# Kernel tuning notes

Measured on AMD Instinct MI355X. Metric: run time of the kernel, lower is better.

## Reference

```python
import jax, jax.numpy as jnp
import numpy as np


def lstm_encode(x, Wih, Whh, b):
    """x: [S, T, F] -> final hidden state [S, H]. PyTorch LSTM gate order (i, f, g, o)."""
    S = x.shape[0]
    H = Whh.shape[1]

    def step(carry, xt):
        h, c = carry
        z = xt @ Wih.T + h @ Whh.T + b  # [S, 4H]
        i, f, g, o = jnp.split(z, 4, axis=-1)
        c = jax.nn.sigmoid(f) * c + jax.nn.sigmoid(i) * jnp.tanh(g)
        h = jax.nn.sigmoid(o) * jnp.tanh(c)
        return (h, c), None

    init = (jnp.zeros((S, H), x.dtype), jnp.zeros((S, H), x.dtype))
    (h, _), _ = jax.lax.scan(step, init, jnp.swapaxes(x, 0, 1))
    return h


def gatv2(h, Ws, Wd, a, bias):
    """Dense GATv2 on batched fully-connected graphs (no self loops).
    h: [G, N, Hin]; Ws, Wd: [nh, Hin, O]; a: [nh, O]; bias: [nh, O] -> [G, N, nh, O].
    Graph is fully connected (all i != j), so edge-softmax == dense row softmax
    with the diagonal masked out; this is the efficient dense form of the
    gather / LeakyReLU / edge-softmax / scatter pattern in DGL's GATv2Conv."""
    nh = Ws.shape[0]
    N = h.shape[1]
    self_mask = jnp.eye(N, dtype=bool)
    outs = []
    for hd in range(nh):  # small fixed head count; loop caps peak memory
        fs = h @ Ws[hd]  # [G, N, O] source-projected feats (messages)
        fd = h @ Wd[hd]  # [G, N, O] dst-projected feats
        e = jax.nn.leaky_relu(fd[:, :, None, :] + fs[:, None, :, :], 0.2)  # [G, dst, src, O]
        logits = jnp.where(self_mask, -jnp.inf, e @ a[hd])  # [G, dst, src]
        attn = jax.nn.softmax(logits, axis=-1)
        outs.append(jnp.einsum('gds,gso->gdo', attn, fs) + bias[hd])
    return jnp.stack(outs, axis=2)


def cosine(x, y, eps=1e-6):
    xn = x / jnp.maximum(jnp.linalg.norm(x, axis=-1, keepdims=True), eps)
    yn = y / jnp.maximum(jnp.linalg.norm(y, axis=-1, keepdims=True), eps)
    return (xn * yn).sum(-1)


def setup_inputs() -> dict:
    key = jax.random.key(0)
    B, K, T, N, F, H, GH, NH = 16, 4, 64, 128, 16, 32, 32, 8
    ks = jax.random.split(key, 16)

    def rn(k, shape, scale=1.0):
        return jax.random.normal(k, shape, jnp.float32) * scale

    return {
        'anchor': rn(ks[0], (B, T, N, F)),
        'pos': rn(ks[1], (B, T, N, F)),
        'neg': rn(ks[2], (B, K, T, N, F)),
        'hideout': rn(ks[3], (B, 2)),
        'timestep': jax.random.uniform(ks[4], (B, 1), jnp.float32),
        'Wih': rn(ks[5], (4 * H, F), 1.0 / np.sqrt(F)),
        'Whh': rn(ks[6], (4 * H, H), 1.0 / np.sqrt(H)),
        'b_lstm': rn(ks[7], (4 * H,), 0.1),
        'W1s': rn(ks[8], (NH, H, H), 1.0 / np.sqrt(H)),
        'W1d': rn(ks[9], (NH, H, H), 1.0 / np.sqrt(H)),
        'a1': rn(ks[10], (NH, H), 1.0 / np.sqrt(H)),
        'b1': rn(ks[11], (NH, H), 0.1),
        'W2s': rn(ks[12], (1, H, GH), 1.0 / np.sqrt(H)),
        'W2d': rn(ks[13], (1, H, GH), 1.0 / np.sqrt(H)),
        'a2': rn(ks[14], (1, GH), 1.0 / np.sqrt(GH)),
        'b2': rn(ks[15], (1, GH), 0.1),
        'num_agents': 128,
    }


def reference(anchor, pos, neg, hideout, timestep, Wih, Whh, b_lstm,
              W1s, W1d, a1, b1, W2s, W2d, a2, b2, num_agents):
    B, T, N, F = anchor.shape
    K = neg.shape[1]
    H = Whh.shape[1]
    # per-agent time series -> LSTM sequences
    a_seq = jnp.transpose(anchor, (0, 2, 1, 3)).reshape(B * N, T, F)
    p_seq = jnp.transpose(pos, (0, 2, 1, 3)).reshape(B * N, T, F)
    n_seq = jnp.transpose(neg, (0, 1, 3, 2, 4)).reshape(B * K * N, T, F)
    hn = lstm_encode(jnp.concatenate([a_seq, p_seq, n_seq], 0), Wih, Whh, b_lstm)
    hg = hn.reshape(-1, N, H)  # [(2+K)*B, N, H] batched fully-connected graphs
    h1 = gatv2(hg, W1s, W1d, a1, b1).mean(axis=2)  # mean over 8 heads
    h2 = gatv2(h1, W2s, W2d, a2, b2)[:, :, 0, :]   # single head, squeezed
    pooled = h2.mean(axis=1)                        # AvgPooling over nodes
    anchor_res = pooled[:B]
    pos_res = pooled[B:2 * B]
    neg_res = pooled[2 * B:].reshape(B, K, -1)
    sim_pos = cosine(anchor_res, pos_res)[:, None]      # [B, 1]
    sim_neg = cosine(anchor_res[:, None, :], neg_res)   # [B, K]
    all_vecs = jnp.concatenate([sim_neg, sim_pos], axis=1)  # positive last
    contrastive = (-jax.nn.log_softmax(all_vecs, axis=1)[:, -1]).mean()
    res = jnp.concatenate([anchor_res, hideout, timestep], axis=-1)
    return res, contrastive
```

## Files before the change

### kernel.cpp

```cpp
#include <hip/hip_runtime.h>
#include <math.h>


typedef __bf16 bf16x8 __attribute__((ext_vector_type(8)));
typedef float  f32x4  __attribute__((ext_vector_type(4)));
typedef unsigned int u32x4 __attribute__((ext_vector_type(4)));

__device__ __forceinline__ float fast_rcp(float x) { return __builtin_amdgcn_rcpf(x); }
__device__ __forceinline__ float sigm(float x)     { return fast_rcp(1.f + __expf(-x)); }
__device__ __forceinline__ float tanh_fast(float x){ return fmaf(2.f, fast_rcp(1.f + __expf(-2.f * x)), -1.f); }

#define KEEP4(x) asm volatile("" : "+v"(x))

__global__ __launch_bounds__(256, 1) void lstm_mfma_kernel(
    const float* __restrict__ anchor, const float* __restrict__ pos,
    const float* __restrict__ neg, const float* __restrict__ Wih,
    const float* __restrict__ Whh, const float* __restrict__ bias,
    float* __restrict__ hn)
{
    __shared__ unsigned int Hbuf[4][512];
    const int tid  = threadIdx.x;
    const int w    = tid >> 6;
    const int lane = tid & 63;
    const int l15  = lane & 15;
    const int g4   = lane >> 4;
    unsigned int* hb = Hbuf[w];

    #pragma unroll
    for (int i = 0; i < 8; ++i) hb[lane + i * 64] = 0u;

    u32x4 whhH[8], whhL[8], wihH[8];
    float bq[8];
    #pragma unroll
    for (int f = 0; f < 8; ++f) {
        const int G = f >> 1, Hh = f & 1;
        const int c = G * 32 + Hh * 16 + l15;
        bq[f] = bias[c];
        union { u32x4 u; bf16x8 v; } th, tl, ti;
        const float* wr = Whh + c * 32 + g4 * 8;
        #pragma unroll
        for (int i = 0; i < 8; ++i) {
            float wv = wr[i];
            __bf16 hi = (__bf16)wv;
            th.v[i] = hi;
            tl.v[i] = (__bf16)(wv - (float)hi);
        }
        if (g4 < 2) {
            const float* wr2 = Wih + c * 16 + g4 * 8;
            #pragma unroll
            for (int i = 0; i < 8; ++i) ti.v[i] = (__bf16)wr2[i];
        } else {
            #pragma unroll
            for (int i = 0; i < 8; ++i) ti.v[i] = (__bf16)0.f;
        }
        whhH[f] = th.u; whhL[f] = tl.u; wihH[f] = ti.u;
    }
    #pragma unroll
    for (int f = 0; f < 8; ++f) { KEEP4(whhH[f]); KEEP4(whhL[f]); KEEP4(wihH[f]); }

    const int s = blockIdx.x * 64 + w * 16 + l15;
    const float* xbase; int sl;
    if (s < 2048)      { xbase = anchor; sl = s; }
    else if (s < 4096) { xbase = pos;    sl = s - 2048; }
    else               { xbase = neg;    sl = s - 4096; }
    const bool xact = (g4 < 2);
    const float* xp = xbase + (sl >> 7) * 131072 + (sl & 127) * 16 + (xact ? g4 * 8 : 0);

    const float4 z4 = make_float4(0.f, 0.f, 0.f, 0.f);
    float4 xaA = z4, xbA = z4, xaB = z4, xbB = z4;
    if (xact) {
        xaA = *(const float4*)(xp);        xbA = *(const float4*)(xp + 4);
        xaB = *(const float4*)(xp + 2048); xbB = *(const float4*)(xp + 2052);
    }

    float cst[8] = {0,0,0,0,0,0,0,0};
    float hv[8]  = {0,0,0,0,0,0,0,0};

    const int c0  = g4 * 2;
    const int swz = (l15 & 3) << 1;
    const int ro0 = l15 * 32 + ((c0 ^ swz) << 2);
    const int ro1 = l15 * 32 + (((c0 + 1) ^ swz) << 2);

    #define LSTM_STEP(XA, XB)                                                          \
    {                                                                                  \
        bf16x8 ax;                                                                     \
        ax[0]=(__bf16)XA.x; ax[1]=(__bf16)XA.y; ax[2]=(__bf16)XA.z; ax[3]=(__bf16)XA.w;\
        ax[4]=(__bf16)XB.x; ax[5]=(__bf16)XB.y; ax[6]=(__bf16)XB.z; ax[7]=(__bf16)XB.w;\
        uint4 v0 = *(const uint4*)(hb + ro0);                                          \
        uint4 v1 = *(const uint4*)(hb + ro1);                                          \
        union { unsigned int u[4]; bf16x8 v; } ahi;                                    \
        ahi.u[0] = __builtin_amdgcn_perm(v0.y, v0.x, 0x05040100u);                     \
        ahi.u[1] = __builtin_amdgcn_perm(v0.w, v0.z, 0x05040100u);                     \
        ahi.u[2] = __builtin_amdgcn_perm(v1.y, v1.x, 0x05040100u);                     \
        ahi.u[3] = __builtin_amdgcn_perm(v1.w, v1.z, 0x05040100u);                     \
        f32x4 z[8];                                                                    \
        _Pragma("unroll")                                                              \
        for (int f = 0; f < 8; ++f) {                                                  \
            f32x4 a = __builtin_amdgcn_mfma_f32_16x16x32_bf16(                         \
                ax, __builtin_bit_cast(bf16x8, wihH[f]), (f32x4)(0.f), 0, 0, 0);       \
            a = __builtin_amdgcn_mfma_f32_16x16x32_bf16(                               \
                ahi.v, __builtin_bit_cast(bf16x8, whhH[f]), a, 0, 0, 0);               \
            a = __builtin_amdgcn_mfma_f32_16x16x32_bf16(                               \
                ahi.v, __builtin_bit_cast(bf16x8, whhL[f]), a, 0, 0, 0);               \
            z[f] = a;                                                                  \
        }                                                                              \
        _Pragma("unroll")                                                              \
        for (int Hh = 0; Hh < 2; ++Hh) {                                               \
            _Pragma("unroll")                                                          \
            for (int r = 0; r < 4; ++r) {                                              \
                const int idx = Hh * 4 + r;                                            \
                float zi = z[0 + Hh][r] + bq[0 + Hh];                                  \
                float zf = z[2 + Hh][r] + bq[2 + Hh];                                  \
                float zg = z[4 + Hh][r] + bq[4 + Hh];                                  \
                float zo = z[6 + Hh][r] + bq[6 + Hh];                                  \
                float cn = fmaf(sigm(zf), cst[idx], sigm(zi) * tanh_fast(zg));         \
                cst[idx] = cn;                                                         \
                float h = sigm(zo) * tanh_fast(cn);                                    \
                hv[idx] = h;                                                           \
                unsigned int pk = (unsigned int)__builtin_bit_cast(unsigned short,     \
                                                                   (__bf16)h);        \
                const int mm = g4 * 4 + r;                                             \
                const int jw = Hh * 16 + l15;                                          \
                hb[mm * 32 + (((jw >> 2) ^ ((mm & 3) << 1)) << 2) + (jw & 3)] = pk;    \
            }                                                                          \
        }                                                                              \
    }

    for (int t = 0; t < 64; t += 2) {
        float4 cA1 = xaA, cA2 = xbA;
        if (xact && t + 2 < 64) {
            const float* p = xp + (t + 2) * 2048;
            xaA = *(const float4*)(p); xbA = *(const float4*)(p + 4);
        }
        LSTM_STEP(cA1, cA2);

        float4 cB1 = xaB, cB2 = xbB;
        if (xact && t + 3 < 64) {
            const float* p = xp + (t + 3) * 2048;
            xaB = *(const float4*)(p); xbB = *(const float4*)(p + 4);
        }
        LSTM_STEP(cB1, cB2);
    }
    #undef LSTM_STEP

    const int seq0 = blockIdx.x * 64 + w * 16;
    #pragma unroll
    for (int Hh = 0; Hh < 2; ++Hh) {
        #pragma unroll
        for (int r = 0; r < 4; ++r) {
            hn[(seq0 + g4 * 4 + r) * 32 + Hh * 16 + l15] = hv[Hh * 4 + r];
        }
    }
}

__device__ __forceinline__ int fsoff(int n) { return n * 36 + ((n >> 5) << 2); }

__global__ __launch_bounds__(256) void gat1_kernel(
    const float* __restrict__ hn, const float* __restrict__ W1s,
    const float* __restrict__ W1d, const float* __restrict__ a1,
    const float* __restrict__ b1, float* __restrict__ h1heads)
{
    const int g = blockIdx.x >> 4, hd = (blockIdx.x >> 1) & 7, half = blockIdx.x & 1;
    const int dbase = half << 6;
    __shared__ float FSf[128 * 36 + 16];
    __shared__ float FD[64][36];
    __shared__ float AVr[32];
    __shared__ float As06[128];
    __shared__ float Ad06[64];
    const int tid = threadIdx.x;

    if (tid < 32) AVr[tid] = a1[hd * 32 + tid];

    {
        const int o = tid & 31, nb = tid >> 5;
        float wcs[32], wcd[32];
        const float* wsp = W1s + hd * 1024 + o;
        const float* wdp = W1d + hd * 1024 + o;
        #pragma unroll
        for (int k = 0; k < 32; ++k) { wcs[k] = wsp[k * 32]; wcd[k] = wdp[k * 32]; }
        const float* hp = hn + g * 4096 + nb * 512;
        const bool own = (nb >> 2) == half;
        #pragma unroll 1
        for (int n = 0; n < 16; ++n) {
            const int row = nb * 16 + n;
            float a0 = 0.f, a1_ = 0.f, b0 = 0.f, b1_ = 0.f;
            #pragma unroll
            for (int k0 = 0; k0 < 32; k0 += 4) {
                float4 hv = *(const float4*)(hp + n * 32 + k0);
                a0 = fmaf(hv.x, wcs[k0+0], a0); b0 = fmaf(hv.x, wcd[k0+0], b0);
                a1_ = fmaf(hv.y, wcs[k0+1], a1_); b1_ = fmaf(hv.y, wcd[k0+1], b1_);
                a0 = fmaf(hv.z, wcs[k0+2], a0); b0 = fmaf(hv.z, wcd[k0+2], b0);
                a1_ = fmaf(hv.w, wcs[k0+3], a1_); b1_ = fmaf(hv.w, wcd[k0+3], b1_);
            }
            FSf[fsoff(row) + o] = a0 + a1_;
            if (own) FD[row - dbase][o] = b0 + b1_;
        }
    }
    __syncthreads();

    if (tid < 128) {
        float ss = 0.f;
        const float* fr = FSf + fsoff(tid);
        #pragma unroll
        for (int oo = 0; oo < 32; ++oo) {
            int o = (oo + tid) & 31;
            ss = fmaf(AVr[o], fr[o], ss);
        }
        As06[tid] = 0.6f * ss;
    } else if (tid < 192) {
        const int dl = tid - 128;
        float sd = 0.f;
        #pragma unroll
        for (int oo = 0; oo < 32; ++oo) {
            int o = (oo + dl) & 31;
            sd = fmaf(AVr[o], FD[dl][o], sd);
        }
        Ad06[dl] = 0.6f * sd;
    }
    __syncthreads();

    const int dl = tid >> 2, d = dbase + dl, sq = tid & 3, sbase = sq << 5;
    float fdr[32], avs[32];
    #pragma unroll
    for (int c = 0; c < 8; ++c) {
        float4 v = *(const float4*)&FD[dl][c * 4];
        fdr[c*4+0] = v.x; fdr[c*4+1] = v.y; fdr[c*4+2] = v.z; fdr[c*4+3] = v.w;
        float4 wv = *(const float4*)&AVr[c * 4];
        avs[c*4+0] = 0.4f * wv.x; avs[c*4+1] = 0.4f * wv.y;
        avs[c*4+2] = 0.4f * wv.z; avs[c*4+3] = 0.4f * wv.w;
    }
    const float adc = Ad06[dl];

    float Z = 0.f;
    float acc[32];
    #pragma unroll
    for (int o = 0; o < 32; ++o) acc[o] = 0.f;
    #pragma unroll 1
    for (int si = 0; si < 32; ++si) {
        const int s = sbase + si;
        const float* fr = FSf + fsoff(s);
        float4 fa[8];
        #pragma unroll
        for (int c = 0; c < 8; ++c) fa[c] = *(const float4*)(fr + c * 4);
        float c0 = 0.f, c1 = 0.f, c2 = 0.f, c3 = 0.f;
        #pragma unroll
        for (int c = 0; c < 8; ++c) {
            float e0 = fdr[c*4+0] + fa[c].x; c0 = fmaf(avs[c*4+0], __builtin_fabsf(e0), c0);
            float e1 = fdr[c*4+1] + fa[c].y; c1 = fmaf(avs[c*4+1], __builtin_fabsf(e1), c1);
            float e2 = fdr[c*4+2] + fa[c].z; c2 = fmaf(avs[c*4+2], __builtin_fabsf(e2), c2);
            float e3 = fdr[c*4+3] + fa[c].w; c3 = fmaf(avs[c*4+3], __builtin_fabsf(e3), c3);
        }
        float v = adc + As06[s] + ((c0 + c1) + (c2 + c3));
        float e = (s == d) ? 0.f : __expf(v);
        Z += e;
        #pragma unroll
        for (int c = 0; c < 8; ++c) {
            acc[c*4+0] = fmaf(e, fa[c].x, acc[c*4+0]);
            acc[c*4+1] = fmaf(e, fa[c].y, acc[c*4+1]);
            acc[c*4+2] = fmaf(e, fa[c].z, acc[c*4+2]);
            acc[c*4+3] = fmaf(e, fa[c].w, acc[c*4+3]);
        }
    }
    Z += __shfl_xor(Z, 1); Z += __shfl_xor(Z, 2);
    const float rz = fast_rcp(Z);
    #pragma unroll
    for (int o = 0; o < 32; ++o) {
        acc[o] += __shfl_xor(acc[o], 1);
        acc[o] += __shfl_xor(acc[o], 2);
    }

    if (sq == 0) {
        float* dst = h1heads + ((size_t)((g * 8 + hd) * 128 + d)) * 32;
        const float* bp = b1 + hd * 32;
        #pragma unroll
        for (int c = 0; c < 8; ++c) {
            float4 v;
            v.x = fmaf(acc[c*4+0], rz, bp[c*4+0]);
            v.y = fmaf(acc[c*4+1], rz, bp[c*4+1]);
            v.z = fmaf(acc[c*4+2], rz, bp[c*4+2]);
            v.w = fmaf(acc[c*4+3], rz, bp[c*4+3]);
            *(float4*)(dst + c * 4) = v;
        }
    }
}

__global__ __launch_bounds__(256) void gat2_kernel(
    const float* __restrict__ h1heads, const float* __restrict__ W2s,
    const float* __restrict__ W2d, const float* __restrict__ a2,
    const float* __restrict__ b2, float* __restrict__ pooled)
{
    const int g = blockIdx.x;
    __shared__ float HS[128][36];
    __shared__ float FSf[128 * 36 + 16];
    __shared__ float FD[128][36];
    __shared__ float AVr[32];
    __shared__ float As06[128];
    __shared__ float Ad06[128];
    const int tid = threadIdx.x;

    if (tid < 32) AVr[tid] = a2[tid];

    {
        #pragma unroll
        for (int i = 0; i < 4; ++i) {
            int idx4 = i * 256 + tid;
            float sx = 0.f, sy = 0.f, sz = 0.f, sw = 0.f;
            #pragma unroll
            for (int hdd = 0; hdd < 8; ++hdd) {
                const float4* src = (const float4*)(h1heads + (size_t)(g * 8 + hdd) * 4096);
                float4 v = src[idx4];
                sx += v.x; sy += v.y; sz += v.z; sw += v.w;
            }
            int n = idx4 >> 3, k0 = (idx4 & 7) * 4;
            float4 r; r.x = sx * 0.125f; r.y = sy * 0.125f; r.z = sz * 0.125f; r.w = sw * 0.125f;
            *(float4*)&HS[n][k0] = r;
        }
    }
    __syncthreads();

    {
        const int o = tid & 31, nb = tid >> 5;
        float wcs[32], wcd[32];
        const float* wsp = W2s + o;
        const float* wdp = W2d + o;
        #pragma unroll
        for (int k = 0; k < 32; ++k) { wcs[k] = wsp[k * 32]; wcd[k] = wdp[k * 32]; }
        #pragma unroll 1
        for (int n = nb * 16; n < nb * 16 + 16; ++n) {
            float a0 = 0.f, a1_ = 0.f, b0 = 0.f, b1_ = 0.f;
            #pragma unroll
            for (int k0 = 0; k0 < 32; k0 += 4) {
                const float4 hv = *(const float4*)&HS[n][k0];
                a0 = fmaf(hv.x, wcs[k0+0], a0); b0 = fmaf(hv.x, wcd[k0+0], b0);
                a1_ = fmaf(hv.y, wcs[k0+1], a1_); b1_ = fmaf(hv.y, wcd[k0+1], b1_);
                a0 = fmaf(hv.z, wcs[k0+2], a0); b0 = fmaf(hv.z, wcd[k0+2], b0);
                a1_ = fmaf(hv.w, wcs[k0+3], a1_); b1_ = fmaf(hv.w, wcd[k0+3], b1_);
            }
            FSf[fsoff(n) + o] = a0 + a1_;
            FD[n][o] = b0 + b1_;
        }
    }
    __syncthreads();

    if (tid < 128) {
        float ss = 0.f, sd = 0.f;
        const float* fr = FSf + fsoff(tid);
        #pragma unroll
        for (int oo = 0; oo < 32; ++oo) {
            int o = (oo + tid) & 31;
            float a = AVr[o];
            ss = fmaf(a, fr[o], ss);
            sd = fmaf(a, FD[tid][o], sd);
        }
        As06[tid] = 0.6f * ss;
        Ad06[tid] = 0.6f * sd;
    }
    __syncthreads();

    const int d = tid >> 1, sbase = (tid & 1) << 6;
    float fdr[32], avs[32];
    #pragma unroll
    for (int c = 0; c < 8; ++c) {
        float4 v = *(const float4*)&FD[d][c * 4];
        fdr[c*4+0] = v.x; fdr[c*4+1] = v.y; fdr[c*4+2] = v.z; fdr[c*4+3] = v.w;
        float4 wv = *(const float4*)&AVr[c * 4];
        avs[c*4+0] = 0.4f * wv.x; avs[c*4+1] = 0.4f * wv.y;
        avs[c*4+2] = 0.4f * wv.z; avs[c*4+3] = 0.4f * wv.w;
    }
    const float adc = Ad06[d];

    float Z = 0.f;
    float acc[32];
    #pragma unroll
    for (int o = 0; o < 32; ++o) acc[o] = 0.f;
    #pragma unroll 1
    for (int si = 0; si < 64; ++si) {
        const int s = sbase + si;
        const float* fr = FSf + fsoff(s);
        float4 fa[8];
        #pragma unroll
        for (int c = 0; c < 8; ++c) fa[c] = *(const float4*)(fr + c * 4);
        float c0 = 0.f, c1 = 0.f, c2 = 0.f, c3 = 0.f;
        #pragma unroll
        for (int c = 0; c < 8; ++c) {
            float e0 = fdr[c*4+0] + fa[c].x; c0 = fmaf(avs[c*4+0], __builtin_fabsf(e0), c0);
            float e1 = fdr[c*4+1] + fa[c].y; c1 = fmaf(avs[c*4+1], __builtin_fabsf(e1), c1);
            float e2 = fdr[c*4+2] + fa[c].z; c2 = fmaf(avs[c*4+2], __builtin_fabsf(e2), c2);
            float e3 = fdr[c*4+3] + fa[c].w; c3 = fmaf(avs[c*4+3], __builtin_fabsf(e3), c3);
        }
        float v = adc + As06[s] + ((c0 + c1) + (c2 + c3));
        float e = (s == d) ? 0.f : __expf(v);
        Z += e;
        #pragma unroll
        for (int c = 0; c < 8; ++c) {
            acc[c*4+0] = fmaf(e, fa[c].x, acc[c*4+0]);
            acc[c*4+1] = fmaf(e, fa[c].y, acc[c*4+1]);
            acc[c*4+2] = fmaf(e, fa[c].z, acc[c*4+2]);
            acc[c*4+3] = fmaf(e, fa[c].w, acc[c*4+3]);
        }
    }
    Z += __shfl_xor(Z, 1);
    const float rz = fast_rcp(Z);
    #pragma unroll
    for (int o = 0; o < 32; ++o) acc[o] += __shfl_xor(acc[o], 1);

    __syncthreads();
    if ((tid & 1) == 0) {
        #pragma unroll
        for (int c = 0; c < 4; ++c) {
            float4 v;
            v.x = acc[c*4+0] * rz; v.y = acc[c*4+1] * rz;
            v.z = acc[c*4+2] * rz; v.w = acc[c*4+3] * rz;
            *(float4*)&FD[d][c * 4] = v;
        }
    } else {
        #pragma unroll
        for (int c = 4; c < 8; ++c) {
            float4 v;
            v.x = acc[c*4+0] * rz; v.y = acc[c*4+1] * rz;
            v.z = acc[c*4+2] * rz; v.w = acc[c*4+3] * rz;
            *(float4*)&FD[d][c * 4] = v;
        }
    }
    __syncthreads();

    if (tid < 32) {
        float sp = 0.f;
        #pragma unroll 1
        for (int n = 0; n < 128; ++n) sp += FD[n][tid];
        pooled[g * 32 + tid] = fmaf(sp, 1.f / 128.f, b2[tid]);
    }
}

__global__ void final_kernel(const float* __restrict__ pooled,
                             const float* __restrict__ hideout,
                             const float* __restrict__ timestep,
                             float* __restrict__ out)
{
    const int b = threadIdx.x;
    __shared__ float lossArr[16];
    if (b < 16) {
        const float* A  = pooled + b * 32;
        const float* Pv = pooled + (16 + b) * 32;
        float av[32];
        float na = 0.f;
        #pragma unroll
        for (int i = 0; i < 32; ++i) { av[i] = A[i]; na += av[i] * av[i]; }
        float npv = 0.f, dp = 0.f;
        #pragma unroll
        for (int i = 0; i < 32; ++i) { float p = Pv[i]; npv += p * p; dp += av[i] * p; }
        const float eps = 1e-6f;
        const float ia = 1.f / fmaxf(sqrtf(na), eps);
        const float sp = dp * ia / fmaxf(sqrtf(npv), eps);
        float sn[4];
        #pragma unroll
        for (int k = 0; k < 4; ++k) {
            const float* Nv = pooled + (32 + b * 4 + k) * 32;
            float nn = 0.f, dn = 0.f;
            #pragma unroll
            for (int i = 0; i < 32; ++i) { float q = Nv[i]; nn += q * q; dn += av[i] * q; }
            sn[k] = dn * ia / fmaxf(sqrtf(nn), eps);
        }
        float m = sp;
        #pragma unroll
        for (int k = 0; k < 4; ++k) m = fmaxf(m, sn[k]);
        float Z = expf(sp - m);
        #pragma unroll
        for (int k = 0; k < 4; ++k) Z += expf(sn[k] - m);
        lossArr[b] = logf(Z) + m - sp;
        float* r = out + b * 35;
        #pragma unroll
        for (int i = 0; i < 32; ++i) r[i] = av[i];
        r[32] = hideout[b * 2];
        r[33] = hideout[b * 2 + 1];
        r[34] = timestep[b];
    }
    __syncthreads();
    if (b == 0) {
        float s = 0.f;
        #pragma unroll
        for (int i = 0; i < 16; ++i) s += lossArr[i];
        out[560] = s * (1.f / 16.f);
    }
}

extern "C" void kernel_launch(void* const* d_in, const int* in_sizes, int n_in,
                              void* d_out, int out_size, void* d_ws, size_t ws_size,
                              hipStream_t stream) {
    const float* anchor   = (const float*)d_in[0];
    const float* pos      = (const float*)d_in[1];
    const float* neg      = (const float*)d_in[2];
    const float* hideout  = (const float*)d_in[3];
    const float* timestep = (const float*)d_in[4];
    const float* Wih      = (const float*)d_in[5];
    const float* Whh      = (const float*)d_in[6];
    const float* b_lstm   = (const float*)d_in[7];
    const float* W1s      = (const float*)d_in[8];
    const float* W1d      = (const float*)d_in[9];
    const float* a1       = (const float*)d_in[10];
    const float* b1       = (const float*)d_in[11];
    const float* W2s      = (const float*)d_in[12];
    const float* W2d      = (const float*)d_in[13];
    const float* a2       = (const float*)d_in[14];
    const float* b2       = (const float*)d_in[15];
    float* out = (float*)d_out;

    char* ws = (char*)d_ws;
    float* hn      = (float*)(ws);
    float* h1heads = (float*)(ws + 1605632);
    float* pooled  = (float*)(ws + 14188544);

    hipLaunchKernelGGL(lstm_mfma_kernel, dim3(192), dim3(256), 0, stream,
                       anchor, pos, neg, Wih, Whh, b_lstm, hn);
    hipLaunchKernelGGL(gat1_kernel,  dim3(1536), dim3(256), 0, stream,
                       hn, W1s, W1d, a1, b1, h1heads);
    hipLaunchKernelGGL(gat2_kernel,  dim3(96),   dim3(256), 0, stream,
                       h1heads, W2s, W2d, a2, b2, pooled);
    hipLaunchKernelGGL(final_kernel, dim3(1),    dim3(64),  0, stream,
                       pooled, hideout, timestep, out);
}
```

Before: 166.5 us.

## Split LSTM hidden columns across wave pairs and skip unused dst projection in GAT1

The LSTM kernel now gives each 16-sequence group to a pair of waves, each computing half of the hidden units (4 gate tiles instead of 8). The two waves exchange h through a double-buffered shared-memory tile with a block barrier every step, and the grid doubles to 384 blocks. This aims to shorten the per-step serial chain and spread work over more CUs, at the cost of a __syncthreads per timestep. Separately, GAT1 threads that do not own destination rows no longer load W1d or compute the dst projection.

Measured after the change: 162.1 us. -2.7%, faster.

```diff
diff --git a/kernel.cpp b/kernel.cpp
--- a/kernel.cpp
+++ b/kernel.cpp
@@ -18,24 +18,22 @@
     const float* __restrict__ Whh, const float* __restrict__ bias,
     float* __restrict__ hn)
 {
-    __shared__ unsigned int Hbuf[4][512];
+    __shared__ unsigned int Hbuf[2][2][512];
     const int tid  = threadIdx.x;
-    const int w    = tid >> 6;
+    const int pair = tid >> 7;
+    const int wid  = (tid >> 6) & 1;
     const int lane = tid & 63;
     const int l15  = lane & 15;
     const int g4   = lane >> 4;
-    unsigned int* hb = Hbuf[w];
-
-    #pragma unroll
-    for (int i = 0; i < 8; ++i) hb[lane + i * 64] = 0u;
-
-    u32x4 whhH[8], whhL[8], wihH[8];
-    float bq[8];
-    #pragma unroll
-    for (int f = 0; f < 8; ++f) {
-        const int G = f >> 1, Hh = f & 1;
-        const int c = G * 32 + Hh * 16 + l15;
-        bq[f] = bias[c];
+
+    for (int i = tid; i < 2048; i += 256) ((unsigned int*)Hbuf)[i] = 0u;
+
+    u32x4 whhH[4], whhL[4], wihH[4];
+    float bq[4];
+    #pragma unroll
+    for (int G = 0; G < 4; ++G) {
+        const int c = G * 32 + wid * 16 + l15;
+        bq[G] = bias[c];
         union { u32x4 u; bf16x8 v; } th, tl, ti;
         const float* wr = Whh + c * 32 + g4 * 8;
         #pragma unroll
@@ -53,12 +51,12 @@
             #pragma unroll
             for (int i = 0; i < 8; ++i) ti.v[i] = (__bf16)0.f;
         }
-        whhH[f] = th.u; whhL[f] = tl.u; wihH[f] = ti.u;
-    }
-    #pragma unroll
-    for (int f = 0; f < 8; ++f) { KEEP4(whhH[f]); KEEP4(whhL[f]); KEEP4(wihH[f]); }
-
-    const int s = blockIdx.x * 64 + w * 16 + l15;
+        whhH[G] = th.u; whhL[G] = tl.u; wihH[G] = ti.u;
+    }
+    #pragma unroll
+    for (int G = 0; G < 4; ++G) { KEEP4(whhH[G]); KEEP4(whhL[G]); KEEP4(wihH[G]); }
+
+    const int s = blockIdx.x * 32 + pair * 16 + l15;
     const float* xbase; int sl;
     if (s < 2048)      { xbase = anchor; sl = s; }
     else if (s < 4096) { xbase = pos;    sl = s - 2048; }
@@ -73,57 +71,61 @@
         xaB = *(const float4*)(xp + 2048); xbB = *(const float4*)(xp + 2052);
     }
 
-    float cst[8] = {0,0,0,0,0,0,0,0};
-    float hv[8]  = {0,0,0,0,0,0,0,0};
+    float cst[4] = {0,0,0,0};
+    float hv[4]  = {0,0,0,0};
 
     const int c0  = g4 * 2;
     const int swz = (l15 & 3) << 1;
     const int ro0 = l15 * 32 + ((c0 ^ swz) << 2);
     const int ro1 = l15 * 32 + (((c0 + 1) ^ swz) << 2);
+    const int jw  = wid * 16 + l15;
+    unsigned int* buf0 = Hbuf[pair][0];
+    unsigned int* buf1 = Hbuf[pair][1];
+    int cur = 0;
+    __syncthreads();
 
     #define LSTM_STEP(XA, XB)                                                          \
     {                                                                                  \
+        const unsigned int* rb = cur ? buf1 : buf0;                                    \
+        unsigned int*       wb = cur ? buf0 : buf1;                                    \
         bf16x8 ax;                                                                     \
         ax[0]=(__bf16)XA.x; ax[1]=(__bf16)XA.y; ax[2]=(__bf16)XA.z; ax[3]=(__bf16)XA.w;\
         ax[4]=(__bf16)XB.x; ax[5]=(__bf16)XB.y; ax[6]=(__bf16)XB.z; ax[7]=(__bf16)XB.w;\
-        uint4 v0 = *(const uint4*)(hb + ro0);                                          \
-        uint4 v1 = *(const uint4*)(hb + ro1);                                          \
+        uint4 v0 = *(const uint4*)(rb + ro0);                                          \
+        uint4 v1 = *(const uint4*)(rb + ro1);                                          \
         union { unsigned int u[4]; bf16x8 v; } ahi;                                    \
         ahi.u[0] = __builtin_amdgcn_perm(v0.y, v0.x, 0x05040100u);                     \
         ahi.u[1] = __builtin_amdgcn_perm(v0.w, v0.z, 0x05040100u);                     \
         ahi.u[2] = __builtin_amdgcn_perm(v1.y, v1.x, 0x05040100u);                     \
         ahi.u[3] = __builtin_amdgcn_perm(v1.w, v1.z, 0x05040100u);                     \
-        f32x4 z[8];                                                                    \
+        f32x4 z[4];                                                                    \
         _Pragma("unroll")                                                              \
-        for (int f = 0; f < 8; ++f) {                                                  \
+        for (int G = 0; G < 4; ++G) {                                                  \
             f32x4 a = __builtin_amdgcn_mfma_f32_16x16x32_bf16(                         \
-                ax, __builtin_bit_cast(bf16x8, wihH[f]), (f32x4)(0.f), 0, 0, 0);       \
+                ax, __builtin_bit_cast(bf16x8, wihH[G]), (f32x4)(0.f), 0, 0, 0);       \
             a = __builtin_amdgcn_mfma_f32_16x16x32_bf16(                               \
-                ahi.v, __builtin_bit_cast(bf16x8, whhH[f]), a, 0, 0, 0);               \
+                ahi.v, __builtin_bit_cast(bf16x8, whhH[G]), a, 0, 0, 0);               \
             a = __builtin_amdgcn_mfma_f32_16x16x32_bf16(                               \
-                ahi.v, __builtin_bit_cast(bf16x8, whhL[f]), a, 0, 0, 0);               \
-            z[f] = a;                                                                  \
+                ahi.v, __builtin_bit_cast(bf16x8, whhL[G]), a, 0, 0, 0);               \
+            z[G] = a;                                                                  \
         }                                                                              \
         _Pragma("unroll")                                                              \
-        for (int Hh = 0; Hh < 2; ++Hh) {                                               \
-            _Pragma("unroll")                                                          \
-            for (int r = 0; r < 4; ++r) {                                              \
-                const int idx = Hh * 4 + r;                                            \
-                float zi = z[0 + Hh][r] + bq[0 + Hh];                                  \
-                float zf = z[2 + Hh][r] + bq[2 + Hh];                                  \
-                float zg = z[4 + Hh][r] + bq[4 + Hh];                                  \
-                float zo = z[6 + Hh][r] + bq[6 + Hh];                                  \
-                float cn = fmaf(sigm(zf), cst[idx], sigm(zi) * tanh_fast(zg));         \
-                cst[idx] = cn;                                                         \
-                float h = sigm(zo) * tanh_fast(cn);                                    \
-                hv[idx] = h;                                                           \
-                unsigned int pk = (unsigned int)__builtin_bit_cast(unsigned short,     \
-                                                                   (__bf16)h);        \
-                const int mm = g4 * 4 + r;                                             \
-                const int jw = Hh * 16 + l15;                                          \
-                hb[mm * 32 + (((jw >> 2) ^ ((mm & 3) << 1)) << 2) + (jw & 3)] = pk;    \
-            }                                                                          \
+        for (int r = 0; r < 4; ++r) {                                                  \
+            float zi = z[0][r] + bq[0];                                                \
+            float zf = z[1][r] + bq[1];                                                \
+            float zg = z[2][r] + bq[2];                                                \
+            float zo = z[3][r] + bq[3];                                                \
+            float cn = fmaf(sigm(zf), cst[r], sigm(zi) * tanh_fast(zg));               \
+            cst[r] = cn;                                                               \
+            float h = sigm(zo) * tanh_fast(cn);                                        \
+            hv[r] = h;                                                                 \
+            unsigned int pk = (unsigned int)__builtin_bit_cast(unsigned short,         \
+                                                               (__bf16)h);            \
+            const int mm = g4 * 4 + r;                                                 \
+            wb[mm * 32 + (((jw >> 2) ^ ((mm & 3) << 1)) << 2) + (jw & 3)] = pk;        \
         }                                                                              \
+        __syncthreads();                                                               \
+        cur ^= 1;                                                                      \
     }
 
     for (int t = 0; t < 64; t += 2) {
@@ -143,13 +145,10 @@
     }
     #undef LSTM_STEP
 
-    const int seq0 = blockIdx.x * 64 + w * 16;
-    #pragma unroll
-    for (int Hh = 0; Hh < 2; ++Hh) {
-        #pragma unroll
-        for (int r = 0; r < 4; ++r) {
-            hn[(seq0 + g4 * 4 + r) * 32 + Hh * 16 + l15] = hv[Hh * 4 + r];
-        }
+    const int seq0 = blockIdx.x * 32 + pair * 16;
+    #pragma unroll
+    for (int r = 0; r < 4; ++r) {
+        hn[(seq0 + g4 * 4 + r) * 32 + jw] = hv[r];
     }
 }
 
@@ -173,27 +172,47 @@
 
     {
         const int o = tid & 31, nb = tid >> 5;
-        float wcs[32], wcd[32];
+        const bool own = (nb >> 2) == half;
+        float wcs[32];
         const float* wsp = W1s + hd * 1024 + o;
-        const float* wdp = W1d + hd * 1024 + o;
-        #pragma unroll
-        for (int k = 0; k < 32; ++k) { wcs[k] = wsp[k * 32]; wcd[k] = wdp[k * 32]; }
+        #pragma unroll
+        for (int k = 0; k < 32; ++k) wcs[k] = wsp[k * 32];
         const float* hp = hn + g * 4096 + nb * 512;
-        const bool own = (nb >> 2) == half;
-        #pragma unroll 1
-        for (int n = 0; n < 16; ++n) {
-            const int row = nb * 16 + n;
-            float a0 = 0.f, a1_ = 0.f, b0 = 0.f, b1_ = 0.f;
+        if (own) {
+            float wcd[32];
+            const float* wdp = W1d + hd * 1024 + o;
             #pragma unroll
-            for (int k0 = 0; k0 < 32; k0 += 4) {
-                float4 hv = *(const float4*)(hp + n * 32 + k0);
-                a0 = fmaf(hv.x, wcs[k0+0], a0); b0 = fmaf(hv.x, wcd[k0+0], b0);
-                a1_ = fmaf(hv.y, wcs[k0+1], a1_); b1_ = fmaf(hv.y, wcd[k0+1], b1_);
-                a0 = fmaf(hv.z, wcs[k0+2], a0); b0 = fmaf(hv.z, wcd[k0+2], b0);
-                a1_ = fmaf(hv.w, wcs[k0+3], a1_); b1_ = fmaf(hv.w, wcd[k0+3], b1_);
+            for (int k = 0; k < 32; ++k) wcd[k] = wdp[k * 32];
+            #pragma unroll 1
+            for (int n = 0; n < 16; ++n) {
+                const int row = nb * 16 + n;
+                float a0 = 0.f, a1_ = 0.f, b0 = 0.f, b1_ = 0.f;
+                #pragma unroll
+                for (int k0 = 0; k0 < 32; k0 += 4) {
+                    float4 hv = *(const float4*)(hp + n * 32 + k0);
+                    a0 = fmaf(hv.x, wcs[k0+0], a0); b0 = fmaf(hv.x, wcd[k0+0], b0);
+                    a1_ = fmaf(hv.y, wcs[k0+1], a1_); b1_ = fmaf(hv.y, wcd[k0+1], b1_);
+                    a0 = fmaf(hv.z, wcs[k0+2], a0); b0 = fmaf(hv.z, wcd[k0+2], b0);
+                    a1_ = fmaf(hv.w, wcs[k0+3], a1_); b1_ = fmaf(hv.w, wcd[k0+3], b1_);
+                }
+                FSf[fsoff(row) + o] = a0 + a1_;
+                FD[row - dbase][o] = b0 + b1_;
             }
-            FSf[fsoff(row) + o] = a0 + a1_;
-            if (own) FD[row - dbase][o] = b0 + b1_;
+        } else {
+            #pragma unroll 1
+            for (int n = 0; n < 16; ++n) {
+                const int row = nb * 16 + n;
+                float a0 = 0.f, a1_ = 0.f;
+                #pragma unroll
+                for (int k0 = 0; k0 < 32; k0 += 4) {
+                    float4 hv = *(const float4*)(hp + n * 32 + k0);
+                    a0 = fmaf(hv.x, wcs[k0+0], a0);
+                    a1_ = fmaf(hv.y, wcs[k0+1], a1_);
+                    a0 = fmaf(hv.z, wcs[k0+2], a0);
+                    a1_ = fmaf(hv.w, wcs[k0+3], a1_);
+                }
+                FSf[fsoff(row) + o] = a0 + a1_;
+            }
         }
     }
     __syncthreads();
@@ -510,7 +529,7 @@
     float* h1heads = (float*)(ws + 1605632);
     float* pooled  = (float*)(ws + 14188544);
 
-    hipLaunchKernelGGL(lstm_mfma_kernel, dim3(192), dim3(256), 0, stream,
+    hipLaunchKernelGGL(lstm_mfma_kernel, dim3(384), dim3(256), 0, stream,
                        anchor, pos, neg, Wih, Whh, b_lstm, hn);
     hipLaunchKernelGGL(gat1_kernel,  dim3(1536), dim3(256), 0, stream,
                        hn, W1s, W1d, a1, b1, h1heads);
```
